# Optimization experiments

Measured on AMD Instinct MI355X. Metric: run time of the kernel, lower is better.

The kernel has to match this reference:

```python
import jax, jax.numpy as jnp
import numpy as np

N = 8192
D_IN = 64
D_OUT = 64
ALPHA = 0.2  # LeakyReLU negative slope


def setup_inputs() -> dict:
    key = jax.random.key(0)
    ks = jax.random.split(key, 6)
    s = 1.0 / np.sqrt(D_IN)
    return {
        "x": jax.random.normal(ks[0], (1, N, D_IN), dtype=jnp.float32),
        "Wt": jax.random.normal(ks[1], (D_IN, D_OUT), dtype=jnp.float32) * s,
        "a1": jax.random.normal(ks[2], (D_OUT,), dtype=jnp.float32) * s,
        "b1": jnp.zeros((), dtype=jnp.float32),
        "a2": jax.random.normal(ks[3], (D_OUT,), dtype=jnp.float32) * s,
        "b2": jnp.zeros((), dtype=jnp.float32),
    }


def reference(x, Wt, a1, b1, a2, b2):
    # Conv1d(kernel=1, bias=False) == pointwise linear: [1,N,Din] @ [Din,Dout]
    h = jnp.einsum("bni,io->bno", x, Wt)            # seq_fts, [1,N,Dout]
    f1 = jnp.einsum("bno,o->bn", h, a1) + b1        # per-node source score
    f2 = jnp.einsum("bno,o->bn", h, a2) + b2        # per-node target score
    logits = f1[:, :, None] + f2[:, None, :]        # [1,N,N]
    coefs = jax.nn.softmax(jax.nn.leaky_relu(logits, ALPHA), axis=-1)
    ret = jnp.einsum("bij,bjo->bio", coefs, h)      # [1,N,Dout]
    return jax.nn.elu(ret)                           # concat=True -> ELU
```

## Files before the change

kernel.cpp:

```cpp
#include <hip/hip_runtime.h>
#include <math.h>

#define N 8192
#define D 64
#define CHUNKS 512
#define CROWS 16
#define KS 32
#define SLICE 256
#define NQ (2 * N)

typedef unsigned long long u64;

__device__ __forceinline__ unsigned ordered_bits(float v) {
  unsigned u = __float_as_uint(v);
  return u ^ (((int)u >> 31) | 0x80000000u);
}

__global__ __launch_bounds__(256) void k1_gemm(
    const float* __restrict__ x, const float* __restrict__ Wt,
    const float* __restrict__ a1, const float* __restrict__ b1,
    const float* __restrict__ a2, const float* __restrict__ b2,
    float* __restrict__ h, float* __restrict__ f1, float* __restrict__ f2,
    u64* __restrict__ key64, u64* __restrict__ thrkey) {
  __shared__ float WtS[D * D];
  __shared__ float xs[16 * D];
  int t = threadIdx.x;
  int rowBase = blockIdx.x * 16;
  for (int i = t; i < D * D; i += 256) WtS[i] = Wt[i];
  for (int i = t; i < 16 * D; i += 256) xs[i] = x[rowBase * D + i];
  __syncthreads();
  int d = t & 63;
  int w = t >> 6;
  float a1d = a1[d], a2d = a2[d];
  float b1v = b1[0], b2v = b2[0];
  for (int it = 0; it < 4; ++it) {
    int rl = w + it * 4;
    float acc = 0.f;
#pragma unroll
    for (int k = 0; k < D; ++k) acc += xs[rl * D + k] * WtS[k * D + d];
    int grow = rowBase + rl;
    h[grow * D + d] = acc;
    float v1 = acc * a1d;
    float v2 = acc * a2d;
#pragma unroll
    for (int off = 32; off > 0; off >>= 1) {
      v1 += __shfl_xor(v1, off);
      v2 += __shfl_xor(v2, off);
    }
    if (d == 0) {
      float F1 = v1 + b1v;
      float F2 = v2 + b2v;
      f1[grow] = F1;
      f2[grow] = F2;
      key64[grow] = ((u64)ordered_bits(F2) << 13) | (unsigned)grow;
      thrkey[grow] = ((u64)ordered_bits(-F1) << 13);
    }
  }
}

__global__ __launch_bounds__(256) void k2a_count(
    const u64* __restrict__ key64, const u64* __restrict__ thrkey,
    int* __restrict__ part) {
  __shared__ u64 ksl[SLICE];
  int t = threadIdx.x;
  int g = blockIdx.x >> 5;
  int s = blockIdx.x & (KS - 1);
  ksl[t] = key64[s * SLICE + t];
  int q0 = g * 1024 + t;
  u64 qa = (q0 < N) ? key64[q0] : thrkey[q0 - N];
  int q1 = q0 + 256;
  u64 qb = (q1 < N) ? key64[q1] : thrkey[q1 - N];
  int q2 = q0 + 512;
  u64 qc = (q2 < N) ? key64[q2] : thrkey[q2 - N];
  int q3 = q0 + 768;
  u64 qd = (q3 < N) ? key64[q3] : thrkey[q3 - N];
  __syncthreads();
  int c0 = 0, c1 = 0, c2 = 0, c3 = 0;
#pragma unroll 8
  for (int l = 0; l < SLICE; ++l) {
    u64 k = ksl[l];
    c0 += (k < qa) ? 1 : 0;
    c1 += (k < qb) ? 1 : 0;
    c2 += (k < qc) ? 1 : 0;
    c3 += (k < qd) ? 1 : 0;
  }
  int* pb = part + s * NQ;
  pb[q0] = c0;
  pb[q1] = c1;
  pb[q2] = c2;
  pb[q3] = c3;
}

__global__ __launch_bounds__(256) void k2b_reduce(
    const int* __restrict__ part, const float* __restrict__ f2,
    int* __restrict__ perm, float* __restrict__ wsm, float* __restrict__ wbg,
    int* __restrict__ ksplit) {
  int q = blockIdx.x * 256 + threadIdx.x;
  int tot = 0;
#pragma unroll
  for (int s = 0; s < KS; ++s) tot += part[s * NQ + q];
  if (q < N) {
    float v = f2[q];
    perm[tot] = q;
    wsm[tot] = expf(0.2f * v);
    wbg[tot] = expf(v);
  } else {
    ksplit[q - N] = tot;
  }
}

__global__ __launch_bounds__(64) void k3c_scan(
    const float* __restrict__ h, const int* __restrict__ perm,
    const float* __restrict__ wsm, const float* __restrict__ wbg,
    float* __restrict__ Pl, float* __restrict__ Sl,
    float* __restrict__ tot_s, float* __restrict__ tot_b,
    float* __restrict__ pl, float* __restrict__ sl,
    float* __restrict__ tots_sc, float* __restrict__ totb_sc) {
  __shared__ float hs[CROWS * D];
  int c = blockIdx.x;
  int d = threadIdx.x;
  int base = c * CROWS;
  int pj = (d < CROWS) ? perm[base + d] : 0;
  float wSv = (d < CROWS) ? wsm[base + d] : 0.f;
  float wBv = (d < CROWS) ? wbg[base + d] : 0.f;
#pragma unroll
  for (int r = 0; r < CROWS; ++r) {
    int j = __shfl(pj, r);
    hs[r * D + d] = h[(size_t)j * D + d];
  }
  float incS = wSv, incB = wBv;
#pragma unroll
  for (int off = 1; off < CROWS; off <<= 1) {
    float uS = __shfl_up(incS, off);
    float uB = __shfl_up(incB, off);
    if ((d & 63) >= off) {
      incS += uS;
      incB += uB;
    }
  }
  float totS = __shfl(incS, CROWS - 1);
  float totB = __shfl(incB, CROWS - 1);
  if (d < CROWS) {
    pl[base + d] = incS - wSv;
    sl[base + d] = totB - (incB - wBv);
  }
  if (d == 0) {
    tots_sc[c] = totS;
    totb_sc[c] = totB;
  }
  __syncthreads();
  float runP = 0.f;
#pragma unroll
  for (int r = 0; r < CROWS; ++r) {
    Pl[(size_t)(base + r) * D + d] = runP;
    runP += __shfl(wSv, r) * hs[r * D + d];
  }
  tot_s[c * D + d] = runP;
  float runS = 0.f;
#pragma unroll
  for (int r = CROWS - 1; r >= 0; --r) {
    runS += __shfl(wBv, r) * hs[r * D + d];
    Sl[(size_t)(base + r) * D + d] = runS;
  }
  tot_b[c * D + d] = runS;
}

__global__ __launch_bounds__(256) void k3b_offsets(
    const float* __restrict__ tot_s, const float* __restrict__ tot_b,
    const float* __restrict__ tots_sc, const float* __restrict__ totb_sc,
    float* __restrict__ off_s, float* __restrict__ off_b,
    float* __restrict__ poff, float* __restrict__ soff,
    float* __restrict__ Pl, float* __restrict__ Sl,
    float* __restrict__ pl, float* __restrict__ sl) {
  int t = threadIdx.x;
  if (t < 64) {
    int d = t;
    float run = 0.f;
    for (int c = 0; c < CHUNKS; ++c) {
      off_s[c * D + d] = run;
      run += tot_s[c * D + d];
    }
    off_s[CHUNKS * D + d] = run;
    Pl[(size_t)N * D + d] = 0.f;
    Sl[(size_t)N * D + d] = 0.f;
  } else if (t < 128) {
    int d = t - 64;
    float run = 0.f;
    for (int c = CHUNKS - 1; c >= 0; --c) {
      off_b[c * D + d] = run;
      run += tot_b[c * D + d];
    }
    off_b[CHUNKS * D + d] = 0.f * run + 0.f;
  } else if (t == 128) {
    float run = 0.f;
    for (int c = 0; c < CHUNKS; ++c) {
      poff[c] = run;
      run += tots_sc[c];
    }
    poff[CHUNKS] = run;
    pl[N] = 0.f;
  } else if (t == 129) {
    float run = 0.f;
    soff[CHUNKS] = 0.f;
    for (int c = CHUNKS - 1; c >= 0; --c) {
      soff[c] = run;
      run += totb_sc[c];
    }
    sl[N] = 0.f;
  }
  if (t >= 64 && t < 128) {
    int d = t - 64;
    off_b[CHUNKS * D + d] = 0.f;
  }
}

__global__ __launch_bounds__(256) void k4_out(
    const float* __restrict__ f1, const int* __restrict__ ksplit,
    const float* __restrict__ off_s, const float* __restrict__ off_b,
    const float* __restrict__ poff, const float* __restrict__ soff,
    const float* __restrict__ Pl, const float* __restrict__ Sl,
    const float* __restrict__ pl, const float* __restrict__ sl,
    float* __restrict__ out) {
  int g = blockIdx.x * 256 + threadIdx.x;
  int row = g >> 6, d = g & 63;
  float f1v = f1[row];
  int k = ksplit[row];
  int c = k >> 4;
  float e1 = expf(f1v), e2 = expf(0.2f * f1v);
  float Sv = off_b[c * D + d] + Sl[(size_t)k * D + d];
  float Pv = off_s[c * D + d] + Pl[(size_t)k * D + d];
  float num = e1 * Sv + e2 * Pv;
  float den = e1 * (soff[c] + sl[k]) + e2 * (poff[c] + pl[k]);
  float v = num / den;
  out[g] = v > 0.f ? v : expm1f(v);
}

extern "C" void kernel_launch(void* const* d_in, const int* in_sizes, int n_in,
                              void* d_out, int out_size, void* d_ws,
                              size_t ws_size, hipStream_t stream) {
  const float* x = (const float*)d_in[0];
  const float* Wt = (const float*)d_in[1];
  const float* a1 = (const float*)d_in[2];
  const float* b1 = (const float*)d_in[3];
  const float* a2 = (const float*)d_in[4];
  const float* b2 = (const float*)d_in[5];
  float* out = (float*)d_out;

  u64* key64 = (u64*)d_ws;
  u64* thrkey = key64 + N;
  float* ws = (float*)(thrkey + N);
  float* h = ws;          ws += N * D;
  float* f1 = ws;         ws += N;
  float* f2v = ws;        ws += N;
  float* wsm = ws;        ws += N;
  float* wbg = ws;        ws += N;
  int* perm = (int*)ws;   ws += N;
  int* ksplit = (int*)ws; ws += N;
  int* part = (int*)ws;   ws += KS * NQ;
  float* Pl = ws;         ws += (size_t)(N + 1) * D;
  float* Sl = ws;         ws += (size_t)(N + 1) * D;
  float* tot_s = ws;      ws += CHUNKS * D;
  float* tot_b = ws;      ws += CHUNKS * D;
  float* off_s = ws;      ws += (CHUNKS + 1) * D;
  float* off_b = ws;      ws += (CHUNKS + 1) * D;
  float* pl = ws;         ws += (N + 1);
  float* sl = ws;         ws += (N + 1);
  float* tots_sc = ws;    ws += CHUNKS;
  float* totb_sc = ws;    ws += CHUNKS;
  float* poff = ws;       ws += (CHUNKS + 1);
  float* soff = ws;       ws += (CHUNKS + 1);

  k1_gemm<<<N / 16, 256, 0, stream>>>(x, Wt, a1, b1, a2, b2, h, f1, f2v,
                                      key64, thrkey);
  k2a_count<<<16 * KS, 256, 0, stream>>>(key64, thrkey, part);
  k2b_reduce<<<NQ / 256, 256, 0, stream>>>(part, f2v, perm, wsm, wbg, ksplit);
  k3c_scan<<<CHUNKS, 64, 0, stream>>>(h, perm, wsm, wbg, Pl, Sl, tot_s, tot_b,
                                      pl, sl, tots_sc, totb_sc);
  k3b_offsets<<<1, 256, 0, stream>>>(tot_s, tot_b, tots_sc, totb_sc, off_s,
                                     off_b, poff, soff, Pl, Sl, pl, sl);
  k4_out<<<(N * D) / 256, 256, 0, stream>>>(f1, ksplit, off_s, off_b, poff,
                                            soff, Pl, Sl, pl, sl, out);
}
```

Before: 116.0 us.

## Fuse all stages into one cooperative kernel with grid-wide syncs

```diff
diff --git a/kernel.cpp b/kernel.cpp
--- a/kernel.cpp
+++ b/kernel.cpp
@@ -1,12 +1,15 @@
 #include <hip/hip_runtime.h>
+#include <hip/hip_cooperative_groups.h>
 #include <math.h>
+
+namespace cg = cooperative_groups;
 
 #define N 8192
 #define D 64
+#define NB 256
+#define NT 512
 #define CHUNKS 512
 #define CROWS 16
-#define KS 32
-#define SLICE 256
 #define NQ (2 * N)
 
 typedef unsigned long long u64;
@@ -16,268 +19,276 @@
   return u ^ (((int)u >> 31) | 0x80000000u);
 }
 
-__global__ __launch_bounds__(256) void k1_gemm(
-    const float* __restrict__ x, const float* __restrict__ Wt,
-    const float* __restrict__ a1, const float* __restrict__ b1,
-    const float* __restrict__ a2, const float* __restrict__ b2,
-    float* __restrict__ h, float* __restrict__ f1, float* __restrict__ f2,
-    u64* __restrict__ key64, u64* __restrict__ thrkey) {
-  __shared__ float WtS[D * D];
-  __shared__ float xs[16 * D];
-  int t = threadIdx.x;
-  int rowBase = blockIdx.x * 16;
-  for (int i = t; i < D * D; i += 256) WtS[i] = Wt[i];
-  for (int i = t; i < 16 * D; i += 256) xs[i] = x[rowBase * D + i];
-  __syncthreads();
-  int d = t & 63;
-  int w = t >> 6;
-  float a1d = a1[d], a2d = a2[d];
-  float b1v = b1[0], b2v = b2[0];
+struct KArgs {
+  const float *x, *Wt, *a1, *b1, *a2, *b2;
+  float *h, *f1, *f2;
+  u64 *key64, *thrkey;
+  int *perm;
+  float *wsm, *wbg;
+  int *ksplit;
+  float *Pl, *Sl, *tot_s, *tot_b, *pl, *sl, *tots_sc, *totb_sc;
+  float *off_s, *off_b, *poff, *soff;
+  float *out;
+};
+
+union SMem {
+  struct { float WtS[D * D]; float xs[32 * D]; } a;
+  struct { u64 ksl[4096]; int part[8][64]; } b;
+  struct { float sc[NT]; } e;
+};
+
+__global__ __launch_bounds__(NT, 1) void fused(KArgs A) {
+  cg::grid_group grid = cg::this_grid();
+  __shared__ SMem s;
+  const int t = threadIdx.x;
+  const int blk = blockIdx.x;
+  const int lane = t & 63;
+  const int wv = t >> 6;
+
+  {
+    for (int i = t; i < D * D; i += NT) s.a.WtS[i] = A.Wt[i];
+    int rowBase = blk * 32;
+    for (int i = t; i < 32 * D; i += NT) s.a.xs[i] = A.x[rowBase * D + i];
+    __syncthreads();
+    float a1d = A.a1[lane], a2d = A.a2[lane];
+    float b1v = A.b1[0], b2v = A.b2[0];
+#pragma unroll
+    for (int it = 0; it < 4; ++it) {
+      int rl = wv + it * 8;
+      float acc = 0.f;
+#pragma unroll
+      for (int k = 0; k < D; ++k) acc += s.a.xs[rl * D + k] * s.a.WtS[k * D + lane];
+      int grow = rowBase + rl;
+      A.h[grow * D + lane] = acc;
+      float v1 = acc * a1d;
+      float v2 = acc * a2d;
+#pragma unroll
+      for (int off = 32; off > 0; off >>= 1) {
+        v1 += __shfl_xor(v1, off);
+        v2 += __shfl_xor(v2, off);
+      }
+      if (lane == 0) {
+        float F1 = v1 + b1v;
+        float F2 = v2 + b2v;
+        A.f1[grow] = F1;
+        A.f2[grow] = F2;
+        A.key64[grow] = ((u64)ordered_bits(F2) << 13) | (unsigned)grow;
+        A.thrkey[grow] = ((u64)ordered_bits(-F1) << 13);
+      }
+    }
+  }
+  grid.sync();
+
+  {
+    int q = blk * 64 + lane;
+    u64 qk = (q < N) ? A.key64[q] : A.thrkey[q - N];
+    int cnt = 0;
+#pragma unroll
+    for (int half = 0; half < 2; ++half) {
+      __syncthreads();
+      for (int i = t; i < 4096; i += NT) s.b.ksl[i] = A.key64[half * 4096 + i];
+      __syncthreads();
+      const u64* base = s.b.ksl + wv * 512;
+#pragma unroll 8
+      for (int i = 0; i < 512; ++i) cnt += (base[i] < qk) ? 1 : 0;
+    }
+    s.b.part[wv][lane] = cnt;
+    __syncthreads();
+    if (wv == 0) {
+      int tot = 0;
+#pragma unroll
+      for (int j = 0; j < 8; ++j) tot += s.b.part[j][lane];
+      if (q < N) {
+        float v = A.f2[q];
+        A.perm[tot] = q;
+        A.wsm[tot] = expf(0.2f * v);
+        A.wbg[tot] = expf(v);
+      } else {
+        A.ksplit[q - N] = tot;
+      }
+    }
+  }
+  grid.sync();
+
+  if (t < 128) {
+    int cl = t >> 6;
+    int c = blk * 2 + cl;
+    int base = c * CROWS;
+    int dd = lane;
+    int pj = (dd < CROWS) ? A.perm[base + dd] : 0;
+    float wS = (dd < CROWS) ? A.wsm[base + dd] : 0.f;
+    float wB = (dd < CROWS) ? A.wbg[base + dd] : 0.f;
+    float hv[CROWS];
+#pragma unroll
+    for (int r = 0; r < CROWS; ++r) {
+      int j = __shfl(pj, r);
+      hv[r] = A.h[(size_t)j * D + dd];
+    }
+    float incS = wS, incB = wB;
+#pragma unroll
+    for (int off = 1; off < CROWS; off <<= 1) {
+      float uS = __shfl_up(incS, off);
+      float uB = __shfl_up(incB, off);
+      if (dd >= off) { incS += uS; incB += uB; }
+    }
+    float totS = __shfl(incS, CROWS - 1);
+    float totB = __shfl(incB, CROWS - 1);
+    if (dd < CROWS) {
+      A.pl[base + dd] = incS - wS;
+      A.sl[base + dd] = totB - (incB - wB);
+    }
+    if (dd == 0) { A.tots_sc[c] = totS; A.totb_sc[c] = totB; }
+    float runP = 0.f;
+#pragma unroll
+    for (int r = 0; r < CROWS; ++r) {
+      A.Pl[(size_t)(base + r) * D + dd] = runP;
+      runP += __shfl(wS, r) * hv[r];
+    }
+    A.tot_s[c * D + dd] = runP;
+    float runS = 0.f;
+#pragma unroll
+    for (int r = CROWS - 1; r >= 0; --r) {
+      runS += __shfl(wB, r) * hv[r];
+      A.Sl[(size_t)(base + r) * D + dd] = runS;
+    }
+    A.tot_b[c * D + dd] = runS;
+  }
+  grid.sync();
+
+  if (blk < 64) {
+    int dd = blk;
+    float v = A.tot_s[t * D + dd];
+    s.e.sc[t] = v;
+    __syncthreads();
+    float inc = v;
+#pragma unroll
+    for (int off = 1; off < NT; off <<= 1) {
+      float u_ = (t >= off) ? s.e.sc[t - off] : 0.f;
+      __syncthreads();
+      inc += u_;
+      s.e.sc[t] = inc;
+      __syncthreads();
+    }
+    A.off_s[t * D + dd] = inc - v;
+    if (t == NT - 1) A.off_s[CHUNKS * D + dd] = inc;
+    if (t == 0) A.Pl[(size_t)N * D + dd] = 0.f;
+  } else if (blk < 128) {
+    int dd = blk - 64;
+    int rc = (CHUNKS - 1) - t;
+    float v = A.tot_b[rc * D + dd];
+    s.e.sc[t] = v;
+    __syncthreads();
+    float inc = v;
+#pragma unroll
+    for (int off = 1; off < NT; off <<= 1) {
+      float u_ = (t >= off) ? s.e.sc[t - off] : 0.f;
+      __syncthreads();
+      inc += u_;
+      s.e.sc[t] = inc;
+      __syncthreads();
+    }
+    A.off_b[rc * D + dd] = inc - v;
+    if (t == 0) {
+      A.off_b[CHUNKS * D + dd] = 0.f;
+      A.Sl[(size_t)N * D + dd] = 0.f;
+    }
+  } else if (blk == 128) {
+    {
+      float v = A.tots_sc[t];
+      s.e.sc[t] = v;
+      __syncthreads();
+      float inc = v;
+#pragma unroll
+      for (int off = 1; off < NT; off <<= 1) {
+        float u_ = (t >= off) ? s.e.sc[t - off] : 0.f;
+        __syncthreads();
+        inc += u_;
+        s.e.sc[t] = inc;
+        __syncthreads();
+      }
+      A.poff[t] = inc - v;
+      if (t == NT - 1) A.poff[CHUNKS] = inc;
+      if (t == 0) A.pl[N] = 0.f;
+    }
+    __syncthreads();
+    {
+      int rc = (CHUNKS - 1) - t;
+      float v = A.totb_sc[rc];
+      s.e.sc[t] = v;
+      __syncthreads();
+      float inc = v;
+#pragma unroll
+      for (int off = 1; off < NT; off <<= 1) {
+        float u_ = (t >= off) ? s.e.sc[t - off] : 0.f;
+        __syncthreads();
+        inc += u_;
+        s.e.sc[t] = inc;
+        __syncthreads();
+      }
+      A.soff[rc] = inc - v;
+      if (t == 0) {
+        A.soff[CHUNKS] = 0.f;
+        A.sl[N] = 0.f;
+      }
+    }
+  }
+  grid.sync();
+
+#pragma unroll
   for (int it = 0; it < 4; ++it) {
-    int rl = w + it * 4;
-    float acc = 0.f;
-#pragma unroll
-    for (int k = 0; k < D; ++k) acc += xs[rl * D + k] * WtS[k * D + d];
-    int grow = rowBase + rl;
-    h[grow * D + d] = acc;
-    float v1 = acc * a1d;
-    float v2 = acc * a2d;
-#pragma unroll
-    for (int off = 32; off > 0; off >>= 1) {
-      v1 += __shfl_xor(v1, off);
-      v2 += __shfl_xor(v2, off);
-    }
-    if (d == 0) {
-      float F1 = v1 + b1v;
-      float F2 = v2 + b2v;
-      f1[grow] = F1;
-      f2[grow] = F2;
-      key64[grow] = ((u64)ordered_bits(F2) << 13) | (unsigned)grow;
-      thrkey[grow] = ((u64)ordered_bits(-F1) << 13);
-    }
-  }
-}
-
-__global__ __launch_bounds__(256) void k2a_count(
-    const u64* __restrict__ key64, const u64* __restrict__ thrkey,
-    int* __restrict__ part) {
-  __shared__ u64 ksl[SLICE];
-  int t = threadIdx.x;
-  int g = blockIdx.x >> 5;
-  int s = blockIdx.x & (KS - 1);
-  ksl[t] = key64[s * SLICE + t];
-  int q0 = g * 1024 + t;
-  u64 qa = (q0 < N) ? key64[q0] : thrkey[q0 - N];
-  int q1 = q0 + 256;
-  u64 qb = (q1 < N) ? key64[q1] : thrkey[q1 - N];
-  int q2 = q0 + 512;
-  u64 qc = (q2 < N) ? key64[q2] : thrkey[q2 - N];
-  int q3 = q0 + 768;
-  u64 qd = (q3 < N) ? key64[q3] : thrkey[q3 - N];
-  __syncthreads();
-  int c0 = 0, c1 = 0, c2 = 0, c3 = 0;
-#pragma unroll 8
-  for (int l = 0; l < SLICE; ++l) {
-    u64 k = ksl[l];
-    c0 += (k < qa) ? 1 : 0;
-    c1 += (k < qb) ? 1 : 0;
-    c2 += (k < qc) ? 1 : 0;
-    c3 += (k < qd) ? 1 : 0;
-  }
-  int* pb = part + s * NQ;
-  pb[q0] = c0;
-  pb[q1] = c1;
-  pb[q2] = c2;
-  pb[q3] = c3;
-}
-
-__global__ __launch_bounds__(256) void k2b_reduce(
-    const int* __restrict__ part, const float* __restrict__ f2,
-    int* __restrict__ perm, float* __restrict__ wsm, float* __restrict__ wbg,
-    int* __restrict__ ksplit) {
-  int q = blockIdx.x * 256 + threadIdx.x;
-  int tot = 0;
-#pragma unroll
-  for (int s = 0; s < KS; ++s) tot += part[s * NQ + q];
-  if (q < N) {
-    float v = f2[q];
-    perm[tot] = q;
-    wsm[tot] = expf(0.2f * v);
-    wbg[tot] = expf(v);
-  } else {
-    ksplit[q - N] = tot;
-  }
-}
-
-__global__ __launch_bounds__(64) void k3c_scan(
-    const float* __restrict__ h, const int* __restrict__ perm,
-    const float* __restrict__ wsm, const float* __restrict__ wbg,
-    float* __restrict__ Pl, float* __restrict__ Sl,
-    float* __restrict__ tot_s, float* __restrict__ tot_b,
-    float* __restrict__ pl, float* __restrict__ sl,
-    float* __restrict__ tots_sc, float* __restrict__ totb_sc) {
-  __shared__ float hs[CROWS * D];
-  int c = blockIdx.x;
-  int d = threadIdx.x;
-  int base = c * CROWS;
-  int pj = (d < CROWS) ? perm[base + d] : 0;
-  float wSv = (d < CROWS) ? wsm[base + d] : 0.f;
-  float wBv = (d < CROWS) ? wbg[base + d] : 0.f;
-#pragma unroll
-  for (int r = 0; r < CROWS; ++r) {
-    int j = __shfl(pj, r);
-    hs[r * D + d] = h[(size_t)j * D + d];
-  }
-  float incS = wSv, incB = wBv;
-#pragma unroll
-  for (int off = 1; off < CROWS; off <<= 1) {
-    float uS = __shfl_up(incS, off);
-    float uB = __shfl_up(incB, off);
-    if ((d & 63) >= off) {
-      incS += uS;
-      incB += uB;
-    }
-  }
-  float totS = __shfl(incS, CROWS - 1);
-  float totB = __shfl(incB, CROWS - 1);
-  if (d < CROWS) {
-    pl[base + d] = incS - wSv;
-    sl[base + d] = totB - (incB - wBv);
-  }
-  if (d == 0) {
-    tots_sc[c] = totS;
-    totb_sc[c] = totB;
-  }
-  __syncthreads();
-  float runP = 0.f;
-#pragma unroll
-  for (int r = 0; r < CROWS; ++r) {
-    Pl[(size_t)(base + r) * D + d] = runP;
-    runP += __shfl(wSv, r) * hs[r * D + d];
-  }
-  tot_s[c * D + d] = runP;
-  float runS = 0.f;
-#pragma unroll
-  for (int r = CROWS - 1; r >= 0; --r) {
-    runS += __shfl(wBv, r) * hs[r * D + d];
-    Sl[(size_t)(base + r) * D + d] = runS;
-  }
-  tot_b[c * D + d] = runS;
-}
-
-__global__ __launch_bounds__(256) void k3b_offsets(
-    const float* __restrict__ tot_s, const float* __restrict__ tot_b,
-    const float* __restrict__ tots_sc, const float* __restrict__ totb_sc,
-    float* __restrict__ off_s, float* __restrict__ off_b,
-    float* __restrict__ poff, float* __restrict__ soff,
-    float* __restrict__ Pl, float* __restrict__ Sl,
-    float* __restrict__ pl, float* __restrict__ sl) {
-  int t = threadIdx.x;
-  if (t < 64) {
-    int d = t;
-    float run = 0.f;
-    for (int c = 0; c < CHUNKS; ++c) {
-      off_s[c * D + d] = run;
-      run += tot_s[c * D + d];
-    }
-    off_s[CHUNKS * D + d] = run;
-    Pl[(size_t)N * D + d] = 0.f;
-    Sl[(size_t)N * D + d] = 0.f;
-  } else if (t < 128) {
-    int d = t - 64;
-    float run = 0.f;
-    for (int c = CHUNKS - 1; c >= 0; --c) {
-      off_b[c * D + d] = run;
-      run += tot_b[c * D + d];
-    }
-    off_b[CHUNKS * D + d] = 0.f * run + 0.f;
-  } else if (t == 128) {
-    float run = 0.f;
-    for (int c = 0; c < CHUNKS; ++c) {
-      poff[c] = run;
-      run += tots_sc[c];
-    }
-    poff[CHUNKS] = run;
-    pl[N] = 0.f;
-  } else if (t == 129) {
-    float run = 0.f;
-    soff[CHUNKS] = 0.f;
-    for (int c = CHUNKS - 1; c >= 0; --c) {
-      soff[c] = run;
-      run += totb_sc[c];
-    }
-    sl[N] = 0.f;
-  }
-  if (t >= 64 && t < 128) {
-    int d = t - 64;
-    off_b[CHUNKS * D + d] = 0.f;
-  }
-}
-
-__global__ __launch_bounds__(256) void k4_out(
-    const float* __restrict__ f1, const int* __restrict__ ksplit,
-    const float* __restrict__ off_s, const float* __restrict__ off_b,
-    const float* __restrict__ poff, const float* __restrict__ soff,
-    const float* __restrict__ Pl, const float* __restrict__ Sl,
-    const float* __restrict__ pl, const float* __restrict__ sl,
-    float* __restrict__ out) {
-  int g = blockIdx.x * 256 + threadIdx.x;
-  int row = g >> 6, d = g & 63;
-  float f1v = f1[row];
-  int k = ksplit[row];
-  int c = k >> 4;
-  float e1 = expf(f1v), e2 = expf(0.2f * f1v);
-  float Sv = off_b[c * D + d] + Sl[(size_t)k * D + d];
-  float Pv = off_s[c * D + d] + Pl[(size_t)k * D + d];
-  float num = e1 * Sv + e2 * Pv;
-  float den = e1 * (soff[c] + sl[k]) + e2 * (poff[c] + pl[k]);
-  float v = num / den;
-  out[g] = v > 0.f ? v : expm1f(v);
+    int g = blk * NT + t + it * (NB * NT);
+    int row = g >> 6, dd = g & 63;
+    float f1v = A.f1[row];
+    int k = A.ksplit[row];
+    int c = k >> 4;
+    float e1 = expf(f1v), e2 = expf(0.2f * f1v);
+    float Sv = A.off_b[c * D + dd] + A.Sl[(size_t)k * D + dd];
+    float Pv = A.off_s[c * D + dd] + A.Pl[(size_t)k * D + dd];
+    float num = e1 * Sv + e2 * Pv;
+    float den = e1 * (A.soff[c] + A.sl[k]) + e2 * (A.poff[c] + A.pl[k]);
+    float v = num / den;
+    A.out[g] = v > 0.f ? v : expm1f(v);
+  }
 }
 
 extern "C" void kernel_launch(void* const* d_in, const int* in_sizes, int n_in,
                               void* d_out, int out_size, void* d_ws,
                               size_t ws_size, hipStream_t stream) {
-  const float* x = (const float*)d_in[0];
-  const float* Wt = (const float*)d_in[1];
-  const float* a1 = (const float*)d_in[2];
-  const float* b1 = (const float*)d_in[3];
-  const float* a2 = (const float*)d_in[4];
-  const float* b2 = (const float*)d_in[5];
-  float* out = (float*)d_out;
+  KArgs A;
+  A.x = (const float*)d_in[0];
+  A.Wt = (const float*)d_in[1];
+  A.a1 = (const float*)d_in[2];
+  A.b1 = (const float*)d_in[3];
+  A.a2 = (const float*)d_in[4];
+  A.b2 = (const float*)d_in[5];
+  A.out = (float*)d_out;
 
   u64* key64 = (u64*)d_ws;
   u64* thrkey = key64 + N;
   float* ws = (float*)(thrkey + N);
-  float* h = ws;          ws += N * D;
-  float* f1 = ws;         ws += N;
-  float* f2v = ws;        ws += N;
-  float* wsm = ws;        ws += N;
-  float* wbg = ws;        ws += N;
-  int* perm = (int*)ws;   ws += N;
-  int* ksplit = (int*)ws; ws += N;
-  int* part = (int*)ws;   ws += KS * NQ;
-  float* Pl = ws;         ws += (size_t)(N + 1) * D;
-  float* Sl = ws;         ws += (size_t)(N + 1) * D;
-  float* tot_s = ws;      ws += CHUNKS * D;
-  float* tot_b = ws;      ws += CHUNKS * D;
-  float* off_s = ws;      ws += (CHUNKS + 1) * D;
-  float* off_b = ws;      ws += (CHUNKS + 1) * D;
-  float* pl = ws;         ws += (N + 1);
-  float* sl = ws;         ws += (N + 1);
-  float* tots_sc = ws;    ws += CHUNKS;
-  float* totb_sc = ws;    ws += CHUNKS;
-  float* poff = ws;       ws += (CHUNKS + 1);
-  float* soff = ws;       ws += (CHUNKS + 1);
-
-  k1_gemm<<<N / 16, 256, 0, stream>>>(x, Wt, a1, b1, a2, b2, h, f1, f2v,
-                                      key64, thrkey);
-  k2a_count<<<16 * KS, 256, 0, stream>>>(key64, thrkey, part);
-  k2b_reduce<<<NQ / 256, 256, 0, stream>>>(part, f2v, perm, wsm, wbg, ksplit);
-  k3c_scan<<<CHUNKS, 64, 0, stream>>>(h, perm, wsm, wbg, Pl, Sl, tot_s, tot_b,
-                                      pl, sl, tots_sc, totb_sc);
-  k3b_offsets<<<1, 256, 0, stream>>>(tot_s, tot_b, tots_sc, totb_sc, off_s,
-                                     off_b, poff, soff, Pl, Sl, pl, sl);
-  k4_out<<<(N * D) / 256, 256, 0, stream>>>(f1, ksplit, off_s, off_b, poff,
-                                            soff, Pl, Sl, pl, sl, out);
+  A.key64 = key64;
+  A.thrkey = thrkey;
+  A.h = ws;            ws += N * D;
+  A.f1 = ws;           ws += N;
+  A.f2 = ws;           ws += N;
+  A.wsm = ws;          ws += N;
+  A.wbg = ws;          ws += N;
+  A.perm = (int*)ws;   ws += N;
+  A.ksplit = (int*)ws; ws += N;
+  A.Pl = ws;           ws += (size_t)(N + 1) * D;
+  A.Sl = ws;           ws += (size_t)(N + 1) * D;
+  A.tot_s = ws;        ws += CHUNKS * D;
+  A.tot_b = ws;        ws += CHUNKS * D;
+  A.off_s = ws;        ws += (CHUNKS + 1) * D;
+  A.off_b = ws;        ws += (CHUNKS + 1) * D;
+  A.pl = ws;           ws += (N + 1);
+  A.sl = ws;           ws += (N + 1);
+  A.tots_sc = ws;      ws += CHUNKS;
+  A.totb_sc = ws;      ws += CHUNKS;
+  A.poff = ws;         ws += (CHUNKS + 1);
+  A.soff = ws;         ws += (CHUNKS + 1);
+
+  void* kargs[] = {(void*)&A};
+  hipLaunchCooperativeKernel((const void*)fused, dim3(NB), dim3(NT), kargs, 0,
+                             stream);
 }
```

New measurement: 224.3 us. 93.4% more time.

## Fuse rank counting with reduction and scan with offsets via last-block pattern

Applied to the files above, without the earlier changes.

```diff
diff --git a/kernel.cpp b/kernel.cpp
--- a/kernel.cpp
+++ b/kernel.cpp
@@ -5,9 +5,6 @@
 #define D 64
 #define CHUNKS 512
 #define CROWS 16
-#define KS 32
-#define SLICE 256
-#define NQ (2 * N)
 
 typedef unsigned long long u64;
 
@@ -21,35 +18,32 @@
     const float* __restrict__ a1, const float* __restrict__ b1,
     const float* __restrict__ a2, const float* __restrict__ b2,
     float* __restrict__ h, float* __restrict__ f1, float* __restrict__ f2,
-    u64* __restrict__ key64, u64* __restrict__ thrkey) {
-  __shared__ float WtS[D * D];
-  __shared__ float xs[16 * D];
+    u64* __restrict__ key64, u64* __restrict__ thrkey, int* __restrict__ ctr) {
   int t = threadIdx.x;
+  int lane = t & 63, wv = t >> 6;
+  if (blockIdx.x == 0 && t == 0) *ctr = 0;
+  float wcol[D];
+#pragma unroll
+  for (int k = 0; k < D; ++k) wcol[k] = Wt[k * D + lane];
+  float a1d = a1[lane], a2d = a2[lane];
+  float b1v = b1[0], b2v = b2[0];
   int rowBase = blockIdx.x * 16;
-  for (int i = t; i < D * D; i += 256) WtS[i] = Wt[i];
-  for (int i = t; i < 16 * D; i += 256) xs[i] = x[rowBase * D + i];
-  __syncthreads();
-  int d = t & 63;
-  int w = t >> 6;
-  float a1d = a1[d], a2d = a2[d];
-  float b1v = b1[0], b2v = b2[0];
+#pragma unroll
   for (int it = 0; it < 4; ++it) {
-    int rl = w + it * 4;
+    int grow = rowBase + wv + it * 4;
+    float xv = x[grow * D + lane];
     float acc = 0.f;
 #pragma unroll
-    for (int k = 0; k < D; ++k) acc += xs[rl * D + k] * WtS[k * D + d];
-    int grow = rowBase + rl;
-    h[grow * D + d] = acc;
-    float v1 = acc * a1d;
-    float v2 = acc * a2d;
+    for (int k = 0; k < D; ++k) acc += __shfl(xv, k) * wcol[k];
+    h[grow * D + lane] = acc;
+    float v1 = acc * a1d, v2 = acc * a2d;
 #pragma unroll
     for (int off = 32; off > 0; off >>= 1) {
       v1 += __shfl_xor(v1, off);
       v2 += __shfl_xor(v2, off);
     }
-    if (d == 0) {
-      float F1 = v1 + b1v;
-      float F2 = v2 + b2v;
+    if (lane == 0) {
+      float F1 = v1 + b1v, F2 = v2 + b2v;
       f1[grow] = F1;
       f2[grow] = F2;
       key64[grow] = ((u64)ordered_bits(F2) << 13) | (unsigned)grow;
@@ -58,159 +52,155 @@
   }
 }
 
-__global__ __launch_bounds__(256) void k2a_count(
+__global__ __launch_bounds__(512) void k2_count(
     const u64* __restrict__ key64, const u64* __restrict__ thrkey,
-    int* __restrict__ part) {
-  __shared__ u64 ksl[SLICE];
-  int t = threadIdx.x;
-  int g = blockIdx.x >> 5;
-  int s = blockIdx.x & (KS - 1);
-  ksl[t] = key64[s * SLICE + t];
-  int q0 = g * 1024 + t;
-  u64 qa = (q0 < N) ? key64[q0] : thrkey[q0 - N];
-  int q1 = q0 + 256;
-  u64 qb = (q1 < N) ? key64[q1] : thrkey[q1 - N];
-  int q2 = q0 + 512;
-  u64 qc = (q2 < N) ? key64[q2] : thrkey[q2 - N];
-  int q3 = q0 + 768;
-  u64 qd = (q3 < N) ? key64[q3] : thrkey[q3 - N];
-  __syncthreads();
-  int c0 = 0, c1 = 0, c2 = 0, c3 = 0;
-#pragma unroll 8
-  for (int l = 0; l < SLICE; ++l) {
-    u64 k = ksl[l];
-    c0 += (k < qa) ? 1 : 0;
-    c1 += (k < qb) ? 1 : 0;
-    c2 += (k < qc) ? 1 : 0;
-    c3 += (k < qd) ? 1 : 0;
-  }
-  int* pb = part + s * NQ;
-  pb[q0] = c0;
-  pb[q1] = c1;
-  pb[q2] = c2;
-  pb[q3] = c3;
-}
-
-__global__ __launch_bounds__(256) void k2b_reduce(
-    const int* __restrict__ part, const float* __restrict__ f2,
+    const float* __restrict__ f2,
     int* __restrict__ perm, float* __restrict__ wsm, float* __restrict__ wbg,
     int* __restrict__ ksplit) {
-  int q = blockIdx.x * 256 + threadIdx.x;
-  int tot = 0;
-#pragma unroll
-  for (int s = 0; s < KS; ++s) tot += part[s * NQ + q];
-  if (q < N) {
-    float v = f2[q];
-    perm[tot] = q;
-    wsm[tot] = expf(0.2f * v);
-    wbg[tot] = expf(v);
-  } else {
-    ksplit[q - N] = tot;
-  }
-}
-
-__global__ __launch_bounds__(64) void k3c_scan(
+  __shared__ u64 ksl[4096];
+  __shared__ int part[8][64];
+  int t = threadIdx.x, lane = t & 63, wv = t >> 6;
+  int q = blockIdx.x * 64 + lane;
+  u64 qk = (q < N) ? key64[q] : thrkey[q - N];
+  int cnt = 0;
+#pragma unroll
+  for (int half = 0; half < 2; ++half) {
+    __syncthreads();
+    for (int i = t; i < 4096; i += 512) ksl[i] = key64[half * 4096 + i];
+    __syncthreads();
+    const u64* base = ksl + wv * 512;
+#pragma unroll 8
+    for (int i = 0; i < 512; ++i) cnt += (base[i] < qk) ? 1 : 0;
+  }
+  part[wv][lane] = cnt;
+  __syncthreads();
+  if (wv == 0) {
+    int tot = 0;
+#pragma unroll
+    for (int j = 0; j < 8; ++j) tot += part[j][lane];
+    if (q < N) {
+      float v = f2[q];
+      perm[tot] = q;
+      wsm[tot] = expf(0.2f * v);
+      wbg[tot] = expf(v);
+    } else {
+      ksplit[q - N] = tot;
+    }
+  }
+}
+
+__global__ __launch_bounds__(256) void k3_scan(
     const float* __restrict__ h, const int* __restrict__ perm,
     const float* __restrict__ wsm, const float* __restrict__ wbg,
     float* __restrict__ Pl, float* __restrict__ Sl,
+    float* __restrict__ pl, float* __restrict__ sl,
     float* __restrict__ tot_s, float* __restrict__ tot_b,
-    float* __restrict__ pl, float* __restrict__ sl,
-    float* __restrict__ tots_sc, float* __restrict__ totb_sc) {
-  __shared__ float hs[CROWS * D];
-  int c = blockIdx.x;
-  int d = threadIdx.x;
+    float* __restrict__ tots_sc, float* __restrict__ totb_sc,
+    float* __restrict__ off_s, float* __restrict__ off_b,
+    float* __restrict__ poff, float* __restrict__ soff, int* __restrict__ ctr) {
+  int t = threadIdx.x, lane = t & 63, wv = t >> 6;
+  int c = blockIdx.x * 4 + wv;
   int base = c * CROWS;
-  int pj = (d < CROWS) ? perm[base + d] : 0;
-  float wSv = (d < CROWS) ? wsm[base + d] : 0.f;
-  float wBv = (d < CROWS) ? wbg[base + d] : 0.f;
+  int dd = lane;
+  int pj = (dd < CROWS) ? perm[base + dd] : 0;
+  float wS = (dd < CROWS) ? wsm[base + dd] : 0.f;
+  float wB = (dd < CROWS) ? wbg[base + dd] : 0.f;
+  float hv[CROWS];
 #pragma unroll
   for (int r = 0; r < CROWS; ++r) {
     int j = __shfl(pj, r);
-    hs[r * D + d] = h[(size_t)j * D + d];
-  }
-  float incS = wSv, incB = wBv;
+    hv[r] = h[(size_t)j * D + dd];
+  }
+  float incS = wS, incB = wB;
 #pragma unroll
   for (int off = 1; off < CROWS; off <<= 1) {
     float uS = __shfl_up(incS, off);
     float uB = __shfl_up(incB, off);
-    if ((d & 63) >= off) {
-      incS += uS;
-      incB += uB;
-    }
+    if (dd >= off) { incS += uS; incB += uB; }
   }
   float totS = __shfl(incS, CROWS - 1);
   float totB = __shfl(incB, CROWS - 1);
-  if (d < CROWS) {
-    pl[base + d] = incS - wSv;
-    sl[base + d] = totB - (incB - wBv);
-  }
-  if (d == 0) {
-    tots_sc[c] = totS;
-    totb_sc[c] = totB;
-  }
+  if (dd < CROWS) {
+    pl[base + dd] = incS - wS;
+    sl[base + dd] = totB - (incB - wB);
+  }
+  if (dd == 0) { tots_sc[c] = totS; totb_sc[c] = totB; }
+  float runP = 0.f;
+#pragma unroll
+  for (int r = 0; r < CROWS; ++r) {
+    Pl[(size_t)(base + r) * D + dd] = runP;
+    runP += __shfl(wS, r) * hv[r];
+  }
+  tot_s[c * D + dd] = runP;
+  float runS = 0.f;
+#pragma unroll
+  for (int r = CROWS - 1; r >= 0; --r) {
+    runS += __shfl(wB, r) * hv[r];
+    Sl[(size_t)(base + r) * D + dd] = runS;
+  }
+  tot_b[c * D + dd] = runS;
+
+  __threadfence();
   __syncthreads();
-  float runP = 0.f;
-#pragma unroll
-  for (int r = 0; r < CROWS; ++r) {
-    Pl[(size_t)(base + r) * D + d] = runP;
-    runP += __shfl(wSv, r) * hs[r * D + d];
-  }
-  tot_s[c * D + d] = runP;
-  float runS = 0.f;
-#pragma unroll
-  for (int r = CROWS - 1; r >= 0; --r) {
-    runS += __shfl(wBv, r) * hs[r * D + d];
-    Sl[(size_t)(base + r) * D + d] = runS;
-  }
-  tot_b[c * D + d] = runS;
-}
-
-__global__ __launch_bounds__(256) void k3b_offsets(
-    const float* __restrict__ tot_s, const float* __restrict__ tot_b,
-    const float* __restrict__ tots_sc, const float* __restrict__ totb_sc,
-    float* __restrict__ off_s, float* __restrict__ off_b,
-    float* __restrict__ poff, float* __restrict__ soff,
-    float* __restrict__ Pl, float* __restrict__ Sl,
-    float* __restrict__ pl, float* __restrict__ sl) {
-  int t = threadIdx.x;
-  if (t < 64) {
-    int d = t;
+  __shared__ int isLast;
+  if (t == 0) isLast = (atomicAdd(ctr, 1) == (int)gridDim.x - 1);
+  __syncthreads();
+  if (!isLast) return;
+  __threadfence();
+  if (wv == 0) {
     float run = 0.f;
-    for (int c = 0; c < CHUNKS; ++c) {
-      off_s[c * D + d] = run;
-      run += tot_s[c * D + d];
-    }
-    off_s[CHUNKS * D + d] = run;
-    Pl[(size_t)N * D + d] = 0.f;
-    Sl[(size_t)N * D + d] = 0.f;
-  } else if (t < 128) {
-    int d = t - 64;
+    for (int c2 = 0; c2 < CHUNKS; ++c2) {
+      off_s[c2 * D + lane] = run;
+      run += tot_s[c2 * D + lane];
+    }
+    off_s[CHUNKS * D + lane] = run;
+    Pl[(size_t)N * D + lane] = 0.f;
+  } else if (wv == 1) {
     float run = 0.f;
-    for (int c = CHUNKS - 1; c >= 0; --c) {
-      off_b[c * D + d] = run;
-      run += tot_b[c * D + d];
-    }
-    off_b[CHUNKS * D + d] = 0.f * run + 0.f;
-  } else if (t == 128) {
-    float run = 0.f;
-    for (int c = 0; c < CHUNKS; ++c) {
-      poff[c] = run;
-      run += tots_sc[c];
-    }
-    poff[CHUNKS] = run;
-    pl[N] = 0.f;
-  } else if (t == 129) {
-    float run = 0.f;
-    soff[CHUNKS] = 0.f;
-    for (int c = CHUNKS - 1; c >= 0; --c) {
-      soff[c] = run;
-      run += totb_sc[c];
-    }
-    sl[N] = 0.f;
-  }
-  if (t >= 64 && t < 128) {
-    int d = t - 64;
-    off_b[CHUNKS * D + d] = 0.f;
+    for (int c2 = CHUNKS - 1; c2 >= 0; --c2) {
+      off_b[c2 * D + lane] = run;
+      run += tot_b[c2 * D + lane];
+    }
+    off_b[CHUNKS * D + lane] = 0.f;
+    Sl[(size_t)N * D + lane] = 0.f;
+  } else if (wv == 2) {
+    int b8 = lane * 8;
+    float ls = 0.f;
+#pragma unroll
+    for (int i = 0; i < 8; ++i) ls += tots_sc[b8 + i];
+    float inc = ls;
+#pragma unroll
+    for (int off = 1; off < 64; off <<= 1) {
+      float u_ = __shfl_up(inc, off);
+      if (lane >= off) inc += u_;
+    }
+    float run = inc - ls;
+#pragma unroll
+    for (int i = 0; i < 8; ++i) {
+      poff[b8 + i] = run;
+      run += tots_sc[b8 + i];
+    }
+    if (lane == 63) poff[CHUNKS] = run;
+    if (lane == 0) pl[N] = 0.f;
+  } else {
+    int b8 = lane * 8;
+    float ls = 0.f;
+#pragma unroll
+    for (int i = 0; i < 8; ++i) ls += totb_sc[(CHUNKS - 1) - (b8 + i)];
+    float inc = ls;
+#pragma unroll
+    for (int off = 1; off < 64; off <<= 1) {
+      float u_ = __shfl_up(inc, off);
+      if (lane >= off) inc += u_;
+    }
+    float run = inc - ls;
+#pragma unroll
+    for (int i = 0; i < 8; ++i) {
+      int m = b8 + i;
+      soff[(CHUNKS - 1) - m] = run;
+      run += totb_sc[(CHUNKS - 1) - m];
+    }
+    if (lane == 0) { soff[CHUNKS] = 0.f; sl[N] = 0.f; }
   }
 }
 
@@ -222,13 +212,13 @@
     const float* __restrict__ pl, const float* __restrict__ sl,
     float* __restrict__ out) {
   int g = blockIdx.x * 256 + threadIdx.x;
-  int row = g >> 6, d = g & 63;
+  int row = g >> 6, dd = g & 63;
   float f1v = f1[row];
   int k = ksplit[row];
   int c = k >> 4;
   float e1 = expf(f1v), e2 = expf(0.2f * f1v);
-  float Sv = off_b[c * D + d] + Sl[(size_t)k * D + d];
-  float Pv = off_s[c * D + d] + Pl[(size_t)k * D + d];
+  float Sv = off_b[c * D + dd] + Sl[(size_t)k * D + dd];
+  float Pv = off_s[c * D + dd] + Pl[(size_t)k * D + dd];
   float num = e1 * Sv + e2 * Pv;
   float den = e1 * (soff[c] + sl[k]) + e2 * (poff[c] + pl[k]);
   float v = num / den;
@@ -256,7 +246,7 @@
   float* wbg = ws;        ws += N;
   int* perm = (int*)ws;   ws += N;
   int* ksplit = (int*)ws; ws += N;
-  int* part = (int*)ws;   ws += KS * NQ;
+  int* ctr = (int*)ws;    ws += 64;
   float* Pl = ws;         ws += (size_t)(N + 1) * D;
   float* Sl = ws;         ws += (size_t)(N + 1) * D;
   float* tot_s = ws;      ws += CHUNKS * D;
@@ -271,13 +261,12 @@
   float* soff = ws;       ws += (CHUNKS + 1);
 
   k1_gemm<<<N / 16, 256, 0, stream>>>(x, Wt, a1, b1, a2, b2, h, f1, f2v,
-                                      key64, thrkey);
-  k2a_count<<<16 * KS, 256, 0, stream>>>(key64, thrkey, part);
-  k2b_reduce<<<NQ / 256, 256, 0, stream>>>(part, f2v, perm, wsm, wbg, ksplit);
-  k3c_scan<<<CHUNKS, 64, 0, stream>>>(h, perm, wsm, wbg, Pl, Sl, tot_s, tot_b,
-                                      pl, sl, tots_sc, totb_sc);
-  k3b_offsets<<<1, 256, 0, stream>>>(tot_s, tot_b, tots_sc, totb_sc, off_s,
-                                     off_b, poff, soff, Pl, Sl, pl, sl);
+                                      key64, thrkey, ctr);
+  k2_count<<<(2 * N) / 64, 512, 0, stream>>>(key64, thrkey, f2v, perm, wsm,
+                                             wbg, ksplit);
+  k3_scan<<<CHUNKS / 4, 256, 0, stream>>>(h, perm, wsm, wbg, Pl, Sl, pl, sl,
+                                          tot_s, tot_b, tots_sc, totb_sc,
+                                          off_s, off_b, poff, soff, ctr);
   k4_out<<<(N * D) / 256, 256, 0, stream>>>(f1, ksplit, off_s, off_b, poff,
                                             soff, Pl, Sl, pl, sl, out);
 }
```

After: 123.7 us. 6.6% more time.

## Parallelize chunk-offset scans across blocks and drop shared memory in GEMM/scan

Applied to the files above, without the earlier changes.

```diff
diff --git a/kernel.cpp b/kernel.cpp
--- a/kernel.cpp
+++ b/kernel.cpp
@@ -22,34 +22,30 @@
     const float* __restrict__ a2, const float* __restrict__ b2,
     float* __restrict__ h, float* __restrict__ f1, float* __restrict__ f2,
     u64* __restrict__ key64, u64* __restrict__ thrkey) {
-  __shared__ float WtS[D * D];
-  __shared__ float xs[16 * D];
   int t = threadIdx.x;
+  int lane = t & 63, wv = t >> 6;
+  float wcol[D];
+#pragma unroll
+  for (int k = 0; k < D; ++k) wcol[k] = Wt[k * D + lane];
+  float a1d = a1[lane], a2d = a2[lane];
+  float b1v = b1[0], b2v = b2[0];
   int rowBase = blockIdx.x * 16;
-  for (int i = t; i < D * D; i += 256) WtS[i] = Wt[i];
-  for (int i = t; i < 16 * D; i += 256) xs[i] = x[rowBase * D + i];
-  __syncthreads();
-  int d = t & 63;
-  int w = t >> 6;
-  float a1d = a1[d], a2d = a2[d];
-  float b1v = b1[0], b2v = b2[0];
+#pragma unroll
   for (int it = 0; it < 4; ++it) {
-    int rl = w + it * 4;
+    int grow = rowBase + wv + it * 4;
+    float xv = x[grow * D + lane];
     float acc = 0.f;
 #pragma unroll
-    for (int k = 0; k < D; ++k) acc += xs[rl * D + k] * WtS[k * D + d];
-    int grow = rowBase + rl;
-    h[grow * D + d] = acc;
-    float v1 = acc * a1d;
-    float v2 = acc * a2d;
+    for (int k = 0; k < D; ++k) acc += __shfl(xv, k) * wcol[k];
+    h[grow * D + lane] = acc;
+    float v1 = acc * a1d, v2 = acc * a2d;
 #pragma unroll
     for (int off = 32; off > 0; off >>= 1) {
       v1 += __shfl_xor(v1, off);
       v2 += __shfl_xor(v2, off);
     }
-    if (d == 0) {
-      float F1 = v1 + b1v;
-      float F2 = v2 + b2v;
+    if (lane == 0) {
+      float F1 = v1 + b1v, F2 = v2 + b2v;
       f1[grow] = F1;
       f2[grow] = F2;
       key64[grow] = ((u64)ordered_bits(F2) << 13) | (unsigned)grow;
@@ -109,108 +105,142 @@
   }
 }
 
-__global__ __launch_bounds__(64) void k3c_scan(
+__global__ __launch_bounds__(256) void k3_scan(
     const float* __restrict__ h, const int* __restrict__ perm,
     const float* __restrict__ wsm, const float* __restrict__ wbg,
     float* __restrict__ Pl, float* __restrict__ Sl,
+    float* __restrict__ pl, float* __restrict__ sl,
     float* __restrict__ tot_s, float* __restrict__ tot_b,
-    float* __restrict__ pl, float* __restrict__ sl,
     float* __restrict__ tots_sc, float* __restrict__ totb_sc) {
-  __shared__ float hs[CROWS * D];
-  int c = blockIdx.x;
-  int d = threadIdx.x;
+  int t = threadIdx.x, lane = t & 63, wv = t >> 6;
+  int c = blockIdx.x * 4 + wv;
   int base = c * CROWS;
-  int pj = (d < CROWS) ? perm[base + d] : 0;
-  float wSv = (d < CROWS) ? wsm[base + d] : 0.f;
-  float wBv = (d < CROWS) ? wbg[base + d] : 0.f;
+  int dd = lane;
+  int pj = (dd < CROWS) ? perm[base + dd] : 0;
+  float wS = (dd < CROWS) ? wsm[base + dd] : 0.f;
+  float wB = (dd < CROWS) ? wbg[base + dd] : 0.f;
+  float hv[CROWS];
 #pragma unroll
   for (int r = 0; r < CROWS; ++r) {
     int j = __shfl(pj, r);
-    hs[r * D + d] = h[(size_t)j * D + d];
-  }
-  float incS = wSv, incB = wBv;
+    hv[r] = h[(size_t)j * D + dd];
+  }
+  float incS = wS, incB = wB;
 #pragma unroll
   for (int off = 1; off < CROWS; off <<= 1) {
     float uS = __shfl_up(incS, off);
     float uB = __shfl_up(incB, off);
-    if ((d & 63) >= off) {
-      incS += uS;
-      incB += uB;
-    }
+    if (dd >= off) { incS += uS; incB += uB; }
   }
   float totS = __shfl(incS, CROWS - 1);
   float totB = __shfl(incB, CROWS - 1);
-  if (d < CROWS) {
-    pl[base + d] = incS - wSv;
-    sl[base + d] = totB - (incB - wBv);
-  }
-  if (d == 0) {
-    tots_sc[c] = totS;
-    totb_sc[c] = totB;
-  }
-  __syncthreads();
+  if (dd < CROWS) {
+    pl[base + dd] = incS - wS;
+    sl[base + dd] = totB - (incB - wB);
+  }
+  if (dd == 0) { tots_sc[c] = totS; totb_sc[c] = totB; }
   float runP = 0.f;
 #pragma unroll
   for (int r = 0; r < CROWS; ++r) {
-    Pl[(size_t)(base + r) * D + d] = runP;
-    runP += __shfl(wSv, r) * hs[r * D + d];
-  }
-  tot_s[c * D + d] = runP;
+    Pl[(size_t)(base + r) * D + dd] = runP;
+    runP += __shfl(wS, r) * hv[r];
+  }
+  tot_s[c * D + dd] = runP;
   float runS = 0.f;
 #pragma unroll
   for (int r = CROWS - 1; r >= 0; --r) {
-    runS += __shfl(wBv, r) * hs[r * D + d];
-    Sl[(size_t)(base + r) * D + d] = runS;
-  }
-  tot_b[c * D + d] = runS;
-}
-
-__global__ __launch_bounds__(256) void k3b_offsets(
+    runS += __shfl(wB, r) * hv[r];
+    Sl[(size_t)(base + r) * D + dd] = runS;
+  }
+  tot_b[c * D + dd] = runS;
+}
+
+__global__ __launch_bounds__(512) void k3b_offsets(
     const float* __restrict__ tot_s, const float* __restrict__ tot_b,
     const float* __restrict__ tots_sc, const float* __restrict__ totb_sc,
     float* __restrict__ off_s, float* __restrict__ off_b,
     float* __restrict__ poff, float* __restrict__ soff,
     float* __restrict__ Pl, float* __restrict__ Sl,
     float* __restrict__ pl, float* __restrict__ sl) {
+  __shared__ float sc[512];
   int t = threadIdx.x;
-  if (t < 64) {
-    int d = t;
-    float run = 0.f;
-    for (int c = 0; c < CHUNKS; ++c) {
-      off_s[c * D + d] = run;
-      run += tot_s[c * D + d];
-    }
-    off_s[CHUNKS * D + d] = run;
-    Pl[(size_t)N * D + d] = 0.f;
-    Sl[(size_t)N * D + d] = 0.f;
-  } else if (t < 128) {
-    int d = t - 64;
-    float run = 0.f;
-    for (int c = CHUNKS - 1; c >= 0; --c) {
-      off_b[c * D + d] = run;
-      run += tot_b[c * D + d];
-    }
-    off_b[CHUNKS * D + d] = 0.f * run + 0.f;
-  } else if (t == 128) {
-    float run = 0.f;
-    for (int c = 0; c < CHUNKS; ++c) {
-      poff[c] = run;
-      run += tots_sc[c];
-    }
-    poff[CHUNKS] = run;
-    pl[N] = 0.f;
-  } else if (t == 129) {
-    float run = 0.f;
-    soff[CHUNKS] = 0.f;
-    for (int c = CHUNKS - 1; c >= 0; --c) {
-      soff[c] = run;
-      run += totb_sc[c];
-    }
-    sl[N] = 0.f;
-  }
-  if (t >= 64 && t < 128) {
-    int d = t - 64;
-    off_b[CHUNKS * D + d] = 0.f;
+  int blk = blockIdx.x;
+  if (blk < 64) {
+    int dd = blk;
+    float v = tot_s[t * D + dd];
+    sc[t] = v;
+    __syncthreads();
+    float inc = v;
+#pragma unroll
+    for (int off = 1; off < 512; off <<= 1) {
+      float u_ = (t >= off) ? sc[t - off] : 0.f;
+      __syncthreads();
+      inc += u_;
+      sc[t] = inc;
+      __syncthreads();
+    }
+    off_s[t * D + dd] = inc - v;
+    if (t == 511) off_s[CHUNKS * D + dd] = inc;
+    if (t == 0) Pl[(size_t)N * D + dd] = 0.f;
+  } else if (blk < 128) {
+    int dd = blk - 64;
+    int rc = 511 - t;
+    float v = tot_b[rc * D + dd];
+    sc[t] = v;
+    __syncthreads();
+    float inc = v;
+#pragma unroll
+    for (int off = 1; off < 512; off <<= 1) {
+      float u_ = (t >= off) ? sc[t - off] : 0.f;
+      __syncthreads();
+      inc += u_;
+      sc[t] = inc;
+      __syncthreads();
+    }
+    off_b[rc * D + dd] = inc - v;
+    if (t == 0) {
+      off_b[CHUNKS * D + dd] = 0.f;
+      Sl[(size_t)N * D + dd] = 0.f;
+    }
+  } else {
+    {
+      float v = tots_sc[t];
+      sc[t] = v;
+      __syncthreads();
+      float inc = v;
+#pragma unroll
+      for (int off = 1; off < 512; off <<= 1) {
+        float u_ = (t >= off) ? sc[t - off] : 0.f;
+        __syncthreads();
+        inc += u_;
+        sc[t] = inc;
+        __syncthreads();
+      }
+      poff[t] = inc - v;
+      if (t == 511) poff[CHUNKS] = inc;
+      if (t == 0) pl[N] = 0.f;
+    }
+    __syncthreads();
+    {
+      int rc = 511 - t;
+      float v = totb_sc[rc];
+      sc[t] = v;
+      __syncthreads();
+      float inc = v;
+#pragma unroll
+      for (int off = 1; off < 512; off <<= 1) {
+        float u_ = (t >= off) ? sc[t - off] : 0.f;
+        __syncthreads();
+        inc += u_;
+        sc[t] = inc;
+        __syncthreads();
+      }
+      soff[rc] = inc - v;
+      if (t == 0) {
+        soff[CHUNKS] = 0.f;
+        sl[N] = 0.f;
+      }
+    }
   }
 }
 
@@ -222,13 +252,13 @@
     const float* __restrict__ pl, const float* __restrict__ sl,
     float* __restrict__ out) {
   int g = blockIdx.x * 256 + threadIdx.x;
-  int row = g >> 6, d = g & 63;
+  int row = g >> 6, dd = g & 63;
   float f1v = f1[row];
   int k = ksplit[row];
   int c = k >> 4;
   float e1 = expf(f1v), e2 = expf(0.2f * f1v);
-  float Sv = off_b[c * D + d] + Sl[(size_t)k * D + d];
-  float Pv = off_s[c * D + d] + Pl[(size_t)k * D + d];
+  float Sv = off_b[c * D + dd] + Sl[(size_t)k * D + dd];
+  float Pv = off_s[c * D + dd] + Pl[(size_t)k * D + dd];
   float num = e1 * Sv + e2 * Pv;
   float den = e1 * (soff[c] + sl[k]) + e2 * (poff[c] + pl[k]);
   float v = num / den;
@@ -274,10 +304,10 @@
                                       key64, thrkey);
   k2a_count<<<16 * KS, 256, 0, stream>>>(key64, thrkey, part);
   k2b_reduce<<<NQ / 256, 256, 0, stream>>>(part, f2v, perm, wsm, wbg, ksplit);
-  k3c_scan<<<CHUNKS, 64, 0, stream>>>(h, perm, wsm, wbg, Pl, Sl, tot_s, tot_b,
-                                      pl, sl, tots_sc, totb_sc);
-  k3b_offsets<<<1, 256, 0, stream>>>(tot_s, tot_b, tots_sc, totb_sc, off_s,
-                                     off_b, poff, soff, Pl, Sl, pl, sl);
+  k3_scan<<<CHUNKS / 4, 256, 0, stream>>>(h, perm, wsm, wbg, Pl, Sl, pl, sl,
+                                          tot_s, tot_b, tots_sc, totb_sc);
+  k3b_offsets<<<129, 512, 0, stream>>>(tot_s, tot_b, tots_sc, totb_sc, off_s,
+                                       off_b, poff, soff, Pl, Sl, pl, sl);
   k4_out<<<(N * D) / 256, 256, 0, stream>>>(f1, ksplit, off_s, off_b, poff,
                                             soff, Pl, Sl, pl, sl, out);
 }
```

Measured after the change: 99.47 us, median of 2. 1.17x faster.
